# Performance work log

Hardware: AMD Instinct MI355X
Metric: run time of the kernel (lower is better)

Reference implementation:

```python
import jax, jax.numpy as jnp
import numpy as np

B, N, C = 4, 2048, 1024
H = 16
HD = C // H
SCALE = HD ** -0.5


def setup_inputs() -> dict:
    key = jax.random.key(0)
    ks = jax.random.split(key, 5)
    s = 0.02
    return {
        "x": jax.random.normal(ks[0], (B, N, C), dtype=jnp.float32),
        "w_qkv": jax.random.normal(ks[1], (C, 3 * C), dtype=jnp.float32) * s,
        "b_qkv": jnp.zeros((3 * C,), dtype=jnp.float32),
        "w_proj": jax.random.normal(ks[2], (C, C), dtype=jnp.float32) * s,
        "b_proj": jnp.zeros((C,), dtype=jnp.float32),
    }


def reference(x, w_qkv, b_qkv, w_proj, b_proj):
    b, n, c = x.shape
    qkv = x @ w_qkv + b_qkv                       # [b, n, 3c]
    qkv = qkv.reshape(b, n, 3, H, HD)
    qkv = jnp.transpose(qkv, (2, 0, 3, 1, 4))     # [3, b, h, n, hd]
    q, k, v = qkv[0], qkv[1], qkv[2]
    attn = jnp.einsum("bhqd,bhkd->bhqk", q, k) * SCALE
    attn = jax.nn.softmax(attn, axis=-1)
    out = jnp.einsum("bhqk,bhkd->bhqd", attn, v)  # [b, h, n, hd]
    out = jnp.transpose(out, (0, 2, 1, 3)).reshape(b, n, c)
    return out @ w_proj + b_proj
```

## Files before the change

kernel.cpp:

```cpp
#include <hip/hip_runtime.h>
#include <cstdint>
#include <cstddef>


typedef __attribute__((ext_vector_type(8))) short short8;
typedef __attribute__((ext_vector_type(4))) float f32x4;
typedef _Float16 half4 __attribute__((ext_vector_type(4)));

#if __has_builtin(__builtin_amdgcn_exp2f)
#define EXP2F(x) __builtin_amdgcn_exp2f(x)
#else
#define EXP2F(x) __expf((x) * 0.69314718056f)
#endif

__device__ __forceinline__ short f2bf(float x) {
  unsigned u = __builtin_bit_cast(unsigned, x);
  u += 0x7fffu + ((u >> 16) & 1u);
  return (short)(u >> 16);
}

__device__ __forceinline__ unsigned pkh(float a, float b) {
  auto h = __builtin_amdgcn_cvt_pkrtz(a, b);
  return __builtin_bit_cast(unsigned, h);
}

__device__ __forceinline__ void async16(const void* g, void* l) {
  __builtin_amdgcn_global_load_lds(
      (const __attribute__((address_space(1))) unsigned*)g,
      (__attribute__((address_space(3))) unsigned*)l, 16, 0, 0);
}


__global__ __launch_bounds__(256) void convert_kernel(const float* __restrict__ in,
                                                      short* __restrict__ out) {
  int i = blockIdx.x * 256 + threadIdx.x;
  const float4* p = (const float4*)in + (size_t)i * 2;
  float4 a = p[0], b = p[1];
  short8 r;
  r[0] = f2bf(a.x); r[1] = f2bf(a.y); r[2] = f2bf(a.z); r[3] = f2bf(a.w);
  r[4] = f2bf(b.x); r[5] = f2bf(b.y); r[6] = f2bf(b.z); r[7] = f2bf(b.w);
  *((short8*)out + i) = r;
}

__global__ __launch_bounds__(256) void wtrans_kernel(const float* __restrict__ in,
                                                     short* __restrict__ out,
                                                     int K, int N) {
  __shared__ float tile[32][33];
  int n0 = blockIdx.x * 32, k0 = blockIdx.y * 32;
  int tx = threadIdx.x, ty = threadIdx.y;
  for (int r = ty; r < 32; r += 8)
    tile[r][tx] = in[(size_t)(k0 + r) * N + n0 + tx];
  __syncthreads();
  for (int r = ty; r < 32; r += 8)
    out[(size_t)(n0 + r) * K + k0 + tx] = f2bf(tile[tx][r]);
}


template <int MODE>
__global__ __launch_bounds__(256) void gemm_kernel(
    const short* __restrict__ A, const short* __restrict__ Bt,
    const float* __restrict__ bias, int Nn,
    short* __restrict__ qb, short* __restrict__ kb, short* __restrict__ vtb,
    float* __restrict__ outp) {
  constexpr int K = 1024;
  __shared__ __align__(16) short As[128 * 32];
  __shared__ __align__(16) short Bs[128 * 32];
  const int tid = threadIdx.x, wave = tid >> 6, lane = tid & 63;
  const int quad = lane >> 4, l16 = lane & 15;
  const int m0 = blockIdx.y * 128, n0 = blockIdx.x * 128;
  const int wrow = (wave >> 1) * 64, wcol = (wave & 1) * 64;

  const int str = lane >> 2;
  const int sgc = ((lane & 3) ^ ((lane >> 3) & 3)) * 8;
  const short* Ag = A + (size_t)(m0 + str) * K + sgc;
  const short* Bg = Bt + (size_t)(n0 + str) * K + sgc;

  const int fsw = (l16 >> 1) & 3;

  f32x4 acc[4][4] = {};

  for (int k0 = 0; k0 < K; k0 += 32) {
#pragma unroll
    for (int i = 0; i < 2; ++i) {
      int c = wave * 2 + i;
      async16(Ag + (size_t)c * 16 * K + k0, (char*)As + c * 1024);
      async16(Bg + (size_t)c * 16 * K + k0, (char*)Bs + c * 1024);
    }
    __syncthreads();
    short8 af[4], bf[4];
#pragma unroll
    for (int t = 0; t < 4; ++t) {
      af[t] = *(const short8*)&As[(wrow + t * 16 + l16) * 32 + ((quad ^ fsw) << 3)];
      bf[t] = *(const short8*)&Bs[(wcol + t * 16 + l16) * 32 + ((quad ^ fsw) << 3)];
    }
#pragma unroll
    for (int mt = 0; mt < 4; ++mt)
#pragma unroll
      for (int nt = 0; nt < 4; ++nt)
        acc[mt][nt] = __builtin_amdgcn_mfma_f32_16x16x32_bf16(af[mt], bf[nt],
                                                              acc[mt][nt], 0, 0, 0);
    __syncthreads();
  }

  if (MODE == 0) {
#pragma unroll
    for (int mt = 0; mt < 4; ++mt) {
      int row0 = m0 + wrow + mt * 16 + quad * 4;
      int b = row0 >> 11, n = row0 & 2047;
#pragma unroll
      for (int nt = 0; nt < 4; ++nt) {
        int col = n0 + wcol + nt * 16 + l16;
        float bv = bias[col];
        float v0 = acc[mt][nt][0] + bv, v1 = acc[mt][nt][1] + bv;
        float v2 = acc[mt][nt][2] + bv, v3 = acc[mt][nt][3] + bv;
        int which = col >> 10;
        int h = (col >> 6) & 15;
        int d = col & 63;
        size_t bh = (size_t)(b * 16 + h);
        if (which == 0) {
          const float qs = 0.18033688f;
          size_t base = (bh * 2048 + n) * 64 + d;
          qb[base]       = f2bf(v0 * qs);
          qb[base + 64]  = f2bf(v1 * qs);
          qb[base + 128] = f2bf(v2 * qs);
          qb[base + 192] = f2bf(v3 * qs);
        } else if (which == 1) {
          size_t base = (bh * 2048 + n) * 64 + d;
          kb[base]       = f2bf(v0);
          kb[base + 64]  = f2bf(v1);
          kb[base + 128] = f2bf(v2);
          kb[base + 192] = f2bf(v3);
        } else {
          uint2 pk;
          pk.x = pkh(v0, v1);
          pk.y = pkh(v2, v3);
          *(uint2*)&vtb[(bh * 64 + d) * 2048 + n] = pk;
        }
      }
    }
  } else {
#pragma unroll
    for (int mt = 0; mt < 4; ++mt) {
      int row0 = m0 + wrow + mt * 16 + quad * 4;
#pragma unroll
      for (int nt = 0; nt < 4; ++nt) {
        int col = n0 + wcol + nt * 16 + l16;
        float bv = bias[col];
        outp[(size_t)row0 * Nn + col]       = acc[mt][nt][0] + bv;
        outp[(size_t)(row0 + 1) * Nn + col] = acc[mt][nt][1] + bv;
        outp[(size_t)(row0 + 2) * Nn + col] = acc[mt][nt][2] + bv;
        outp[(size_t)(row0 + 3) * Nn + col] = acc[mt][nt][3] + bv;
      }
    }
  }
}


__global__ __launch_bounds__(256, 4) void attn_kernel(
    const short* __restrict__ qb, const short* __restrict__ kb,
    const short* __restrict__ vtb, short* __restrict__ ob) {
  __shared__ __align__(16) short Ks[2][64 * 64];
  __shared__ __align__(16) short Vs[2][64 * 64];
  __shared__ __align__(16) float Ls[4][32];
  const int tid = threadIdx.x, wave = tid >> 6, lane = tid & 63;
  const int quad = lane >> 4, l16 = lane & 15;
  const int q0 = blockIdx.x * 128;
  const int bh = blockIdx.y;
  const short* Qg = qb + (size_t)bh * (2048 * 64);
  const short* Kg = kb + (size_t)bh * (2048 * 64);
  const short* Vg = vtb + (size_t)bh * (64 * 2048);

  short8 qf[2][2];
#pragma unroll
  for (int qt = 0; qt < 2; ++qt)
#pragma unroll
    for (int kc = 0; kc < 2; ++kc)
      qf[qt][kc] = *(const short8*)
          &Qg[(size_t)(q0 + wave * 32 + qt * 16 + l16) * 64 + kc * 32 + quad * 8];

  const int str = lane >> 3;
  const int sgc = ((lane & 7) ^ (str & 7)) * 8;
  const int fsw = l16 & 7;
  const int c0 = wave * 2, c1 = wave * 2 + 1;

  async16(Kg + (size_t)(c0 * 8 + str) * 64 + sgc, (char*)Ks[0] + c0 * 1024);
  async16(Kg + (size_t)(c1 * 8 + str) * 64 + sgc, (char*)Ks[0] + c1 * 1024);
  async16(Vg + (size_t)(c0 * 8 + str) * 2048 + sgc, (char*)Vs[0] + c0 * 1024);
  async16(Vg + (size_t)(c1 * 8 + str) * 2048 + sgc, (char*)Vs[0] + c1 * 1024);

  float lsum[2] = {0.f, 0.f};
  f32x4 oacc[2][4] = {};

  for (int t = 0; t < 32; ++t) {
    __syncthreads();

    int kvn = (t + 1) * 64;
    if (kvn < 2048) {
      char* kd = (char*)Ks[(t + 1) & 1];
      char* vd = (char*)Vs[(t + 1) & 1];
      async16(Kg + (size_t)(kvn + c0 * 8 + str) * 64 + sgc, kd + c0 * 1024);
      async16(Kg + (size_t)(kvn + c1 * 8 + str) * 64 + sgc, kd + c1 * 1024);
      async16(Vg + (size_t)(c0 * 8 + str) * 2048 + kvn + sgc, vd + c0 * 1024);
      async16(Vg + (size_t)(c1 * 8 + str) * 2048 + kvn + sgc, vd + c1 * 1024);
    }
    const short* Kst = Ks[t & 1];
    const short* Vst = Vs[t & 1];

    f32x4 sacc[2][4] = {};
#pragma unroll
    for (int kc = 0; kc < 2; ++kc) {
      short8 kf[4];
#pragma unroll
      for (int kvt = 0; kvt < 4; ++kvt)
        kf[kvt] = *(const short8*)
            &Kst[(kvt * 16 + l16) * 64 + (((kc * 4 + quad) ^ fsw) << 3)];
#pragma unroll
      for (int kvt = 0; kvt < 4; ++kvt)
#pragma unroll
        for (int qt = 0; qt < 2; ++qt)
          sacc[qt][kvt] = __builtin_amdgcn_mfma_f32_16x16x32_bf16(
              kf[kvt], qf[qt][kc], sacc[qt][kvt], 0, 0, 0);
    }

#pragma unroll
    for (int kvt = 0; kvt < 4; ++kvt) {
      half4 pfr[2];
#pragma unroll
      for (int qt = 0; qt < 2; ++qt) {
        float p0 = EXP2F(sacc[qt][kvt][0]);
        float p1 = EXP2F(sacc[qt][kvt][1]);
        float p2 = EXP2F(sacc[qt][kvt][2]);
        float p3 = EXP2F(sacc[qt][kvt][3]);
        lsum[qt] += (p0 + p1) + (p2 + p3);
        uint2 w;
        w.x = pkh(p0, p1);
        w.y = pkh(p2, p3);
        pfr[qt] = __builtin_bit_cast(half4, w);
      }
      const int vcol = (((kvt * 2 + (quad >> 1)) ^ fsw) << 3) + (quad & 1) * 4;
#pragma unroll
      for (int nt = 0; nt < 4; ++nt) {
        uint2 vr = *(const uint2*)&Vst[(nt * 16 + l16) * 64 + vcol];
        half4 vfr = __builtin_bit_cast(half4, vr);
#pragma unroll
        for (int qt = 0; qt < 2; ++qt)
          oacc[qt][nt] = __builtin_amdgcn_mfma_f32_16x16x16f16(
              pfr[qt], vfr, oacc[qt][nt], 0, 0, 0);
      }
    }
  }

#pragma unroll
  for (int qt = 0; qt < 2; ++qt) {
    float v = lsum[qt];
    v += __shfl_xor(v, 16, 64);
    v += __shfl_xor(v, 32, 64);
    if (quad == 0) Ls[wave][qt * 16 + l16] = v;
  }
  __asm__ volatile("s_waitcnt lgkmcnt(0)" ::: "memory");
  __builtin_amdgcn_wave_barrier();

  const int b = bh >> 4, h = bh & 15;
#pragma unroll
  for (int qt = 0; qt < 2; ++qt) {
    float4 lr = *(const float4*)&Ls[wave][qt * 16 + quad * 4];
    float inv0 = 1.f / lr.x, inv1 = 1.f / lr.y, inv2 = 1.f / lr.z, inv3 = 1.f / lr.w;
#pragma unroll
    for (int nt = 0; nt < 4; ++nt) {
      int d = nt * 16 + l16;
      int qbase = q0 + wave * 32 + qt * 16 + quad * 4;
      size_t obase = ((size_t)(b * 2048 + qbase)) * 1024 + h * 64 + d;
      ob[obase]        = f2bf(oacc[qt][nt][0] * inv0);
      ob[obase + 1024] = f2bf(oacc[qt][nt][1] * inv1);
      ob[obase + 2048] = f2bf(oacc[qt][nt][2] * inv2);
      ob[obase + 3072] = f2bf(oacc[qt][nt][3] * inv3);
    }
  }
}


extern "C" void kernel_launch(void* const* d_in, const int* in_sizes, int n_in,
                              void* d_out, int out_size, void* d_ws, size_t ws_size,
                              hipStream_t stream) {
  const float* x      = (const float*)d_in[0];
  const float* w_qkv  = (const float*)d_in[1];
  const float* b_qkv  = (const float*)d_in[2];
  const float* w_proj = (const float*)d_in[3];
  const float* b_proj = (const float*)d_in[4];
  float* out = (float*)d_out;

  short* xs     = (short*)d_ws;
  short* wqkvT  = xs + (size_t)8192 * 1024;
  short* wprojT = wqkvT + (size_t)3072 * 1024;
  short* qb     = wprojT + (size_t)1024 * 1024;
  short* kb     = qb + (size_t)64 * 2048 * 64;
  short* vtb    = kb + (size_t)64 * 2048 * 64;
  short* aob    = vtb + (size_t)64 * 2048 * 64;

  convert_kernel<<<dim3(4096), 256, 0, stream>>>(x, xs);
  wtrans_kernel<<<dim3(96, 32), dim3(32, 8), 0, stream>>>(w_qkv, wqkvT, 1024, 3072);
  wtrans_kernel<<<dim3(32, 32), dim3(32, 8), 0, stream>>>(w_proj, wprojT, 1024, 1024);

  gemm_kernel<0><<<dim3(24, 64), 256, 0, stream>>>(xs, wqkvT, b_qkv, 3072,
                                                   qb, kb, vtb, nullptr);
  attn_kernel<<<dim3(16, 64), 256, 0, stream>>>(qb, kb, vtb, aob);
  gemm_kernel<1><<<dim3(8, 64), 256, 0, stream>>>(aob, wprojT, b_proj, 1024,
                                                  nullptr, nullptr, nullptr, out);
}
```

Measured before the change: 282.8 us.

## Pre-tile V in attention-ready layout and replace LDS row-sum exchange with shuffles

The QKV epilogue now writes V transposed into per-64-key tiles with a rotated dword layout, so each attention tile is one contiguous 8KB chunk. The attention kernel loads each tile with linear async copies and reads V fragments as two dword LDS loads that are meant to avoid bank conflicts. K and V pointers are advanced incrementally instead of recomputing addresses. The final softmax normalizer is broadcast with lane shuffles instead of going through shared memory. V writes in the GEMM epilogue become scattered 4-byte stores, which may cost bandwidth there.

```diff
diff --git a/kernel.cpp b/kernel.cpp
--- a/kernel.cpp
+++ b/kernel.cpp
@@ -131,10 +131,12 @@
           kb[base + 128] = f2bf(v2);
           kb[base + 192] = f2bf(v3);
         } else {
-          uint2 pk;
-          pk.x = pkh(v0, v1);
-          pk.y = pkh(v2, v3);
-          *(uint2*)&vtb[(bh * 64 + d) * 2048 + n] = pk;
+          int g = (n >> 2) & 15;
+          int dd = (d + 16 * (g & 3)) & 63;
+          unsigned* vd = (unsigned*)vtb + (bh << 16) +
+                         ((n >> 6) * 2048) + (g * 64) + dd;
+          vd[0]    = pkh(v0, v1);
+          vd[1024] = pkh(v2, v3);
         }
       }
     }
@@ -161,14 +163,11 @@
     const short* __restrict__ vtb, short* __restrict__ ob) {
   __shared__ __align__(16) short Ks[2][64 * 64];
   __shared__ __align__(16) short Vs[2][64 * 64];
-  __shared__ __align__(16) float Ls[4][32];
   const int tid = threadIdx.x, wave = tid >> 6, lane = tid & 63;
   const int quad = lane >> 4, l16 = lane & 15;
   const int q0 = blockIdx.x * 128;
   const int bh = blockIdx.y;
   const short* Qg = qb + (size_t)bh * (2048 * 64);
-  const short* Kg = kb + (size_t)bh * (2048 * 64);
-  const short* Vg = vtb + (size_t)bh * (64 * 2048);
 
   short8 qf[2][2];
 #pragma unroll
@@ -181,30 +180,39 @@
   const int str = lane >> 3;
   const int sgc = ((lane & 7) ^ (str & 7)) * 8;
   const int fsw = l16 & 7;
-  const int c0 = wave * 2, c1 = wave * 2 + 1;
-
-  async16(Kg + (size_t)(c0 * 8 + str) * 64 + sgc, (char*)Ks[0] + c0 * 1024);
-  async16(Kg + (size_t)(c1 * 8 + str) * 64 + sgc, (char*)Ks[0] + c1 * 1024);
-  async16(Vg + (size_t)(c0 * 8 + str) * 2048 + sgc, (char*)Vs[0] + c0 * 1024);
-  async16(Vg + (size_t)(c1 * 8 + str) * 2048 + sgc, (char*)Vs[0] + c1 * 1024);
+  const int c0 = wave * 2, c1 = c0 + 1;
+
+  const char* Kp0 = (const char*)(kb + (size_t)bh * (2048 * 64)
+                                  + (size_t)(c0 * 8 + str) * 64 + sgc);
+  const char* Kp1 = Kp0 + 1024;
+  const char* Vp0 = (const char*)vtb + ((size_t)bh << 18) + c0 * 1024 + lane * 16;
+  const char* Vp1 = Vp0 + 1024;
+
+  async16(Kp0, (char*)Ks[0] + c0 * 1024);
+  async16(Kp1, (char*)Ks[0] + c1 * 1024);
+  async16(Vp0, (char*)Vs[0] + c0 * 1024);
+  async16(Vp1, (char*)Vs[0] + c1 * 1024);
+  Kp0 += 8192; Kp1 += 8192; Vp0 += 8192; Vp1 += 8192;
 
   float lsum[2] = {0.f, 0.f};
   f32x4 oacc[2][4] = {};
 
+  const int vsh = l16 + 16 * quad;
+
   for (int t = 0; t < 32; ++t) {
     __syncthreads();
 
-    int kvn = (t + 1) * 64;
-    if (kvn < 2048) {
+    if (t < 31) {
       char* kd = (char*)Ks[(t + 1) & 1];
       char* vd = (char*)Vs[(t + 1) & 1];
-      async16(Kg + (size_t)(kvn + c0 * 8 + str) * 64 + sgc, kd + c0 * 1024);
-      async16(Kg + (size_t)(kvn + c1 * 8 + str) * 64 + sgc, kd + c1 * 1024);
-      async16(Vg + (size_t)(c0 * 8 + str) * 2048 + kvn + sgc, vd + c0 * 1024);
-      async16(Vg + (size_t)(c1 * 8 + str) * 2048 + kvn + sgc, vd + c1 * 1024);
+      async16(Kp0, kd + c0 * 1024);
+      async16(Kp1, kd + c1 * 1024);
+      async16(Vp0, vd + c0 * 1024);
+      async16(Vp1, vd + c1 * 1024);
+      Kp0 += 8192; Kp1 += 8192; Vp0 += 8192; Vp1 += 8192;
     }
     const short* Kst = Ks[t & 1];
-    const short* Vst = Vs[t & 1];
+    const unsigned* VsP = (const unsigned*)Vs[t & 1];
 
     f32x4 sacc[2][4] = {};
 #pragma unroll
@@ -237,10 +245,13 @@
         w.y = pkh(p2, p3);
         pfr[qt] = __builtin_bit_cast(half4, w);
       }
-      const int vcol = (((kvt * 2 + (quad >> 1)) ^ fsw) << 3) + (quad & 1) * 4;
+      const int vbase = (kvt * 4 + quad) * 64;
 #pragma unroll
       for (int nt = 0; nt < 4; ++nt) {
-        uint2 vr = *(const uint2*)&Vst[(nt * 16 + l16) * 64 + vcol];
+        int dd = (nt * 16 + vsh) & 63;
+        uint2 vr;
+        vr.x = VsP[vbase + dd];
+        vr.y = VsP[vbase + dd + 1024];
         half4 vfr = __builtin_bit_cast(half4, vr);
 #pragma unroll
         for (int qt = 0; qt < 2; ++qt)
@@ -250,21 +261,16 @@
     }
   }
 
+  const int b = bh >> 4, h = bh & 15;
 #pragma unroll
   for (int qt = 0; qt < 2; ++qt) {
     float v = lsum[qt];
     v += __shfl_xor(v, 16, 64);
     v += __shfl_xor(v, 32, 64);
-    if (quad == 0) Ls[wave][qt * 16 + l16] = v;
-  }
-  __asm__ volatile("s_waitcnt lgkmcnt(0)" ::: "memory");
-  __builtin_amdgcn_wave_barrier();
-
-  const int b = bh >> 4, h = bh & 15;
-#pragma unroll
-  for (int qt = 0; qt < 2; ++qt) {
-    float4 lr = *(const float4*)&Ls[wave][qt * 16 + quad * 4];
-    float inv0 = 1.f / lr.x, inv1 = 1.f / lr.y, inv2 = 1.f / lr.z, inv3 = 1.f / lr.w;
+    float inv0 = 1.f / __shfl(v, quad * 4 + 0, 64);
+    float inv1 = 1.f / __shfl(v, quad * 4 + 1, 64);
+    float inv2 = 1.f / __shfl(v, quad * 4 + 2, 64);
+    float inv3 = 1.f / __shfl(v, quad * 4 + 3, 64);
 #pragma unroll
     for (int nt = 0; nt < 4; ++nt) {
       int d = nt * 16 + l16;
```

Measured after the change: 285.2 us. About the same (+0.9%).
